# Optimization experiments

Measured on AMD Instinct MI355X. Metric: run time of the kernel, lower is better.

Reference implementation:

```python
import jax, jax.numpy as jnp
import numpy as np

B = 64
L_IN = 4001
L_CONV = 998  # (4001-10)//4 + 1
D = 1000
EPS = 1e-5


def _convlin(x, cw, cb, lw, lb):
    # x: (B,1,4001), cw: (1,1,10), lw: (1000,998)
    y = jax.lax.conv_general_dilated(
        x, cw, window_strides=(4,), padding='VALID',
        dimension_numbers=('NCH', 'OIH', 'NCH')) + cb[None, :, None]  # (B,1,998)
    y = y @ lw.T + lb  # (B,1,1000)
    return jax.nn.relu(y)


def setup_inputs() -> dict:
    key = jax.random.key(0)
    ks = jax.random.split(key, 24)
    f32 = jnp.float32
    inp = {
        'x': jax.random.normal(ks[0], (B, 1, L_IN), dtype=f32),
        'bn_gamma': jnp.ones((L_IN,), f32),
        'bn_beta': jnp.zeros((L_IN,), f32),
        'bn_mean': jax.random.normal(ks[1], (L_IN,), f32) * 0.1,
        'bn_var': jax.random.uniform(ks[2], (L_IN,), f32, 0.5, 1.5),
        'conv_w_q': jax.random.normal(ks[3], (1, 1, 10), f32) * 0.3,
        'conv_b_q': jax.random.normal(ks[4], (1,), f32) * 0.1,
        'lin_w_q': jax.random.normal(ks[5], (D, L_CONV), f32) * (1.0 / np.sqrt(L_CONV)),
        'lin_b_q': jax.random.normal(ks[6], (D,), f32) * 0.02,
        'conv_w_k': jax.random.normal(ks[7], (1, 1, 10), f32) * 0.3,
        'conv_b_k': jax.random.normal(ks[8], (1,), f32) * 0.1,
        'lin_w_k': jax.random.normal(ks[9], (D, L_CONV), f32) * (1.0 / np.sqrt(L_CONV)),
        'lin_b_k': jax.random.normal(ks[10], (D,), f32) * 0.02,
        'conv_w_v': jax.random.normal(ks[11], (1, 1, 10), f32) * 0.3,
        'conv_b_v': jax.random.normal(ks[12], (1,), f32) * 0.1,
        'lin_w_v': jax.random.normal(ks[13], (D, L_CONV), f32) * (1.0 / np.sqrt(L_CONV)),
        'lin_b_v': jax.random.normal(ks[14], (D,), f32) * 0.02,
        'in_proj_w': jax.random.normal(ks[15], (3, 1), f32),
        'in_proj_b': jax.random.normal(ks[16], (3,), f32) * 0.02,
        'out_proj_w': jax.random.normal(ks[17], (1, 1), f32),
        'out_proj_b': jax.random.normal(ks[18], (1,), f32) * 0.02,
        'out_w': jax.random.normal(ks[19], (D, D), f32) * (1.0 / np.sqrt(D)),
        'out_b': jax.random.normal(ks[20], (D,), f32) * 0.02,
    }
    return inp


def reference(x, bn_gamma, bn_beta, bn_mean, bn_var,
              conv_w_q, conv_b_q, lin_w_q, lin_b_q,
              conv_w_k, conv_b_k, lin_w_k, lin_b_k,
              conv_w_v, conv_b_v, lin_w_v, lin_b_v,
              in_proj_w, in_proj_b, out_proj_w, out_proj_b,
              out_w, out_b):
    # BatchNorm1d over last dim (eval mode, running stats); x: (B,1,4001)
    xn = (x - bn_mean[None, None, :]) * jax.lax.rsqrt(bn_var[None, None, :] + EPS)
    xn = xn * bn_gamma[None, None, :] + bn_beta[None, None, :]

    Q = _convlin(xn, conv_w_q, conv_b_q, lin_w_q, lin_b_q)[:, 0, :]  # (B,1000)
    K = _convlin(xn, conv_w_k, conv_b_k, lin_w_k, lin_b_k)[:, 0, :]
    V = _convlin(xn, conv_w_v, conv_b_v, lin_w_v, lin_b_v)[:, 0, :]

    # MHA with embed_dim=1, num_heads=1 -> scalar in-projections, scale = 1
    q = Q * in_proj_w[0, 0] + in_proj_b[0]  # (B,1000)
    k = K * in_proj_w[1, 0] + in_proj_b[1]
    v = V * in_proj_w[2, 0] + in_proj_b[2]

    scores = q[:, :, None] * k[:, None, :]  # (B,1000,1000)
    attn = jax.nn.softmax(scores, axis=-1)
    ctx = jnp.einsum('bqk,bk->bq', attn, v)  # (B,1000)
    ctx = ctx * out_proj_w[0, 0] + out_proj_b[0]

    out = ctx[:, None, :] @ out_w.T + out_b  # (B,1,1000)
    return out
```

## Files before the change

kernel.cpp:

```cpp
#include <hip/hip_runtime.h>
#include <math.h>

#define NB 64
#define LIN 4001
#define LC 998
#define ND 1000
#define EPSBN 1e-5f

#define OFF_CONVT 0u
#define OFF_P     191616u
#define OFF_Q     388224u
#define OFF_KV    452224u
#define OFF_CF    583296u

__global__ __launch_bounds__(256) void k_bnconv(
    const float* __restrict__ x,
    const float* __restrict__ g, const float* __restrict__ be,
    const float* __restrict__ mu, const float* __restrict__ va,
    const float* __restrict__ cwq, const float* __restrict__ cbq,
    const float* __restrict__ cwk, const float* __restrict__ cbk,
    const float* __restrict__ cwv, const float* __restrict__ cbv,
    float* __restrict__ convT)
{
    int j = blockIdx.x * 256 + threadIdx.x;
    int b = blockIdx.y;
    if (j >= LC) return;
    const float* xb = x + (size_t)b * LIN + 4 * j;
    float aq = 0.f, ak = 0.f, av = 0.f;
#pragma unroll
    for (int t = 0; t < 10; ++t) {
        int i = 4 * j + t;
        float s  = g[i] * rsqrtf(va[i] + EPSBN);
        float xn = (xb[t] - mu[i]) * s + be[i];
        aq = fmaf(xn, cwq[t], aq);
        ak = fmaf(xn, cwk[t], ak);
        av = fmaf(xn, cwv[t], av);
    }
    convT[((size_t)0 * LC + j) * 64 + b] = aq + cbq[0];
    convT[((size_t)1 * LC + j) * 64 + b] = ak + cbk[0];
    convT[((size_t)2 * LC + j) * 64 + b] = av + cbv[0];
}

__global__ __launch_bounds__(256) void k_lin(
    const float* __restrict__ convT,
    const float* __restrict__ lwq, const float* __restrict__ lwk,
    const float* __restrict__ lwv,
    float* __restrict__ P)
{
    __shared__ float lds[16384];
    float* ldsC = lds;
    float* ldsW = lds + 8000;
    int tid  = threadIdx.x;
    int lane = tid & 63;
    int w    = tid >> 6;
    int b0   = (lane & 7) << 3;
    int d0   = (lane >> 3) << 3;
    int dgb   = blockIdx.x * 64;
    int which = blockIdx.y;
    int chunk = blockIdx.z;
    int j0 = chunk * 125;
    int jc = (LC - j0 < 125) ? (LC - j0) : 125;
    const float* lw = (which == 0) ? lwq : ((which == 1) ? lwk : lwv);

    {
        const float4* src = (const float4*)(convT + ((size_t)which * LC + j0) * 64);
        float4* dst = (float4*)ldsC;
        for (int t = tid; t < jc * 16; t += 256) dst[t] = src[t];
    }
    for (int idx = tid; idx < 8192; idx += 256) {
        int dd = idx >> 7, jj = idx & 127;
        if (jj < 127) {
            int dg = dgb + dd;
            ldsW[dd * 127 + jj] =
                (dg < ND && jj < jc) ? lw[(size_t)dg * LC + j0 + jj] : 0.f;
        }
    }
    __syncthreads();

    float acc[8][8];
#pragma unroll
    for (int i = 0; i < 8; ++i)
#pragma unroll
        for (int jx = 0; jx < 8; ++jx) acc[i][jx] = 0.f;

    int js = w * 32;
    int je = (jc < js + 32) ? jc : (js + 32);
    for (int jj = js; jj < je; ++jj) {
        float4 c0 = *(const float4*)(ldsC + jj * 64 + b0);
        float4 c1 = *(const float4*)(ldsC + jj * 64 + b0 + 4);
        float cv[8] = {c0.x, c0.y, c0.z, c0.w, c1.x, c1.y, c1.z, c1.w};
        float wv[8];
#pragma unroll
        for (int r = 0; r < 8; ++r) wv[r] = ldsW[(d0 + r) * 127 + jj];
#pragma unroll
        for (int i = 0; i < 8; ++i)
#pragma unroll
            for (int jx = 0; jx < 8; ++jx)
                acc[i][jx] = fmaf(cv[i], wv[jx], acc[i][jx]);
    }

    __syncthreads();
    float* red = lds + w * 4096;
#pragma unroll
    for (int i = 0; i < 8; ++i) {
        *(float4*)(red + (b0 + i) * 64 + d0) =
            make_float4(acc[i][0], acc[i][1], acc[i][2], acc[i][3]);
        *(float4*)(red + (b0 + i) * 64 + d0 + 4) =
            make_float4(acc[i][4], acc[i][5], acc[i][6], acc[i][7]);
    }
    __syncthreads();
    float* Pt = P + ((size_t)(which * 16 + blockIdx.x)) * 4096;
    for (int t = tid; t < 1024; t += 256) {
        float4 a = ((const float4*)lds)[t];
        float4 bq = ((const float4*)(lds + 4096))[t];
        float4 c = ((const float4*)(lds + 8192))[t];
        float4 d = ((const float4*)(lds + 12288))[t];
        atomicAdd(Pt + t * 4 + 0, a.x + bq.x + c.x + d.x);
        atomicAdd(Pt + t * 4 + 1, a.y + bq.y + c.y + d.y);
        atomicAdd(Pt + t * 4 + 2, a.z + bq.z + c.z + d.z);
        atomicAdd(Pt + t * 4 + 3, a.w + bq.w + c.w + d.w);
    }
}

__global__ __launch_bounds__(256) void k_act(
    const float* __restrict__ P,
    const float* __restrict__ lbq, const float* __restrict__ lbk,
    const float* __restrict__ lbv,
    const float* __restrict__ ipw, const float* __restrict__ ipb,
    float* __restrict__ q, float* __restrict__ kv)
{
    int i = blockIdx.x * 256 + threadIdx.x;
    int b = blockIdx.y;
    if (i >= ND) return;
    int it = i >> 6, il = i & 63;
    size_t cell = (size_t)it * 4096 + (b << 6) + il;
    float s0 = P[(0 * 16) * 4096 + cell];
    float s1 = P[(1 * 16) * 4096 + cell];
    float s2 = P[(2 * 16) * 4096 + cell];
    float yq = fmaxf(s0 + lbq[i], 0.f) * ipw[0] + ipb[0];
    float yk = fmaxf(s1 + lbk[i], 0.f) * ipw[1] + ipb[1];
    float yv = fmaxf(s2 + lbv[i], 0.f) * ipw[2] + ipb[2];
    q[(size_t)b * ND + i] = yq;
    kv[(size_t)b * 2048 + 2 * i]     = yk;
    kv[(size_t)b * 2048 + 2 * i + 1] = yv;
}

__global__ __launch_bounds__(256) void k_attn(
    const float* __restrict__ q, const float* __restrict__ kv,
    const float* __restrict__ opw, const float* __restrict__ opb,
    float* __restrict__ cfT)
{
    __shared__ float ldsKV[2048];
    __shared__ float sred[512];
    __shared__ float rmax[4];
    __shared__ float rmin[4];
    int tid  = threadIdx.x;
    int b    = blockIdx.y;
    int half = tid >> 7;
    int ii   = tid & 127;
    int i    = blockIdx.x * 128 + ii;

    {
        const float4* src = (const float4*)(kv + (size_t)b * 2048);
        float4* dst = (float4*)ldsKV;
        for (int t = tid; t < 512; t += 256) dst[t] = src[t];
    }
    __syncthreads();

    float km = -INFINITY, kn = INFINITY;
    const float2* kv2 = (const float2*)ldsKV;
    for (int idx = tid; idx < ND; idx += 256) {
        float2 f = kv2[idx];
        km = fmaxf(km, f.x);
        kn = fminf(kn, f.x);
    }
#pragma unroll
    for (int off = 1; off < 64; off <<= 1) {
        km = fmaxf(km, __shfl_xor(km, off));
        kn = fminf(kn, __shfl_xor(kn, off));
    }
    if ((tid & 63) == 0) { rmax[tid >> 6] = km; rmin[tid >> 6] = kn; }
    __syncthreads();
    km = fmaxf(fmaxf(rmax[0], rmax[1]), fmaxf(rmax[2], rmax[3]));
    kn = fminf(fminf(rmin[0], rmin[1]), fminf(rmin[2], rmin[3]));

    float qi = (i < ND) ? q[(size_t)b * ND + i] : 0.f;
    float m  = (qi >= 0.f) ? qi * km : qi * kn;

    int jbase = half * 500;
    float den = 0.f, num = 0.f;
#pragma unroll 4
    for (int jl = 0; jl < 500; ++jl) {
        float2 f = kv2[jbase + jl];
        float e  = __expf(fmaf(qi, f.x, -m));
        den += e;
        num = fmaf(e, f.y, num);
    }
    sred[tid]       = den;
    sred[256 + tid] = num;
    __syncthreads();
    if (half == 0 && i < ND) {
        float dt  = sred[ii] + sred[128 + ii];
        float nt  = sred[256 + ii] + sred[256 + 128 + ii];
        float ctx = nt / dt;
        cfT[(size_t)i * 64 + b] = ctx * opw[0] + opb[0];
    }
}

__global__ __launch_bounds__(256) void k_out(
    const float* __restrict__ cfT, const float* __restrict__ W,
    const float* __restrict__ outb, float* __restrict__ out)
{
    __shared__ float lds[16384];
    float* ldsC = lds;
    float* ldsW = lds + 8000;
    int tid  = threadIdx.x;
    int lane = tid & 63;
    int w    = tid >> 6;
    int b0   = (lane & 7) << 3;
    int d0   = (lane >> 3) << 3;
    int egb   = blockIdx.x * 64;
    int chunk = blockIdx.y;
    int j0 = chunk * 125;

    {
        const float4* src = (const float4*)(cfT + (size_t)j0 * 64);
        float4* dst = (float4*)ldsC;
        for (int t = tid; t < 125 * 16; t += 256) dst[t] = src[t];
    }
    for (int idx = tid; idx < 8192; idx += 256) {
        int dd = idx >> 7, jj = idx & 127;
        if (jj < 127) {
            int eg = egb + dd;
            ldsW[dd * 127 + jj] =
                (eg < ND && jj < 125) ? W[(size_t)eg * ND + j0 + jj] : 0.f;
        }
    }
    __syncthreads();

    float acc[8][8];
#pragma unroll
    for (int i = 0; i < 8; ++i)
#pragma unroll
        for (int jx = 0; jx < 8; ++jx) acc[i][jx] = 0.f;

    int js = w * 32;
    int je = (125 < js + 32) ? 125 : (js + 32);
    for (int jj = js; jj < je; ++jj) {
        float4 c0 = *(const float4*)(ldsC + jj * 64 + b0);
        float4 c1 = *(const float4*)(ldsC + jj * 64 + b0 + 4);
        float cv[8] = {c0.x, c0.y, c0.z, c0.w, c1.x, c1.y, c1.z, c1.w};
        float wv[8];
#pragma unroll
        for (int r = 0; r < 8; ++r) wv[r] = ldsW[(d0 + r) * 127 + jj];
#pragma unroll
        for (int i = 0; i < 8; ++i)
#pragma unroll
            for (int jx = 0; jx < 8; ++jx)
                acc[i][jx] = fmaf(cv[i], wv[jx], acc[i][jx]);
    }

    __syncthreads();
    float* red = lds + w * 4096;
#pragma unroll
    for (int i = 0; i < 8; ++i) {
        *(float4*)(red + (b0 + i) * 64 + d0) =
            make_float4(acc[i][0], acc[i][1], acc[i][2], acc[i][3]);
        *(float4*)(red + (b0 + i) * 64 + d0 + 4) =
            make_float4(acc[i][4], acc[i][5], acc[i][6], acc[i][7]);
    }
    __syncthreads();
    for (int t = tid; t < 4096; t += 256) {
        int bb = t >> 6, dd = t & 63;
        int eg = egb + dd;
        if (eg < ND) {
            float v = lds[t] + lds[4096 + t] + lds[8192 + t] + lds[12288 + t];
            if (chunk == 0) v += outb[eg];
            atomicAdd(out + (size_t)bb * ND + eg, v);
        }
    }
}

extern "C" void kernel_launch(void* const* d_in, const int* in_sizes, int n_in,
                              void* d_out, int out_size, void* d_ws, size_t ws_size,
                              hipStream_t stream)
{
    const float* x    = (const float*)d_in[0];
    const float* g    = (const float*)d_in[1];
    const float* be   = (const float*)d_in[2];
    const float* mu   = (const float*)d_in[3];
    const float* va   = (const float*)d_in[4];
    const float* cwq  = (const float*)d_in[5];
    const float* cbq  = (const float*)d_in[6];
    const float* lwq  = (const float*)d_in[7];
    const float* lbq  = (const float*)d_in[8];
    const float* cwk  = (const float*)d_in[9];
    const float* cbk  = (const float*)d_in[10];
    const float* lwk  = (const float*)d_in[11];
    const float* lbk  = (const float*)d_in[12];
    const float* cwv  = (const float*)d_in[13];
    const float* cbv  = (const float*)d_in[14];
    const float* lwv  = (const float*)d_in[15];
    const float* lbv  = (const float*)d_in[16];
    const float* ipw  = (const float*)d_in[17];
    const float* ipb  = (const float*)d_in[18];
    const float* opw  = (const float*)d_in[19];
    const float* opb  = (const float*)d_in[20];
    const float* W    = (const float*)d_in[21];
    const float* outb = (const float*)d_in[22];

    float* ws    = (float*)d_ws;
    float* convT = ws + OFF_CONVT;
    float* P     = ws + OFF_P;
    float* q     = ws + OFF_Q;
    float* kv    = ws + OFF_KV;
    float* cfT   = ws + OFF_CF;
    float* out   = (float*)d_out;

    hipMemsetAsync(P, 0, 196608u * sizeof(float), stream);
    hipMemsetAsync(d_out, 0, (size_t)out_size * sizeof(float), stream);

    k_bnconv<<<dim3(4, 64), 256, 0, stream>>>(x, g, be, mu, va,
                                              cwq, cbq, cwk, cbk, cwv, cbv, convT);
    k_lin  <<<dim3(16, 3, 8), 256, 0, stream>>>(convT, lwq, lwk, lwv, P);
    k_act  <<<dim3(4, 64), 256, 0, stream>>>(P, lbq, lbk, lbv, ipw, ipb, q, kv);
    k_attn <<<dim3(8, 64), 256, 0, stream>>>(q, kv, opw, opb, cfT);
    k_out  <<<dim3(16, 8), 256, 0, stream>>>(cfT, W, outb, out);
}
```

Measured before the change: 197.1 us.

## Replace atomic split-K reductions with per-chunk partial buffers and finish kernels

Both GEMMs now share a tile routine that writes per-chunk partial sums to workspace instead of using atomicAdd, with the split-K chunk size lowered to 96 and the chunk count raised to 11. The bias-add and chunk sum are done in k_act and in a new k_fin kernel, so the two memsets are dropped. Weight loads are vectorised to float2, and the attention kernel splits the key loop four ways over 64 queries per block, doubling the grid. This removes atomic contention and memset launches at the cost of one extra kernel launch and more workspace traffic.

```diff
diff --git a/kernel.cpp b/kernel.cpp
--- a/kernel.cpp
+++ b/kernel.cpp
@@ -7,11 +7,16 @@
 #define ND 1000
 #define EPSBN 1e-5f
 
+#define CK 96
+#define NCH_LIN 11
+#define NCH_OUT 11
+
 #define OFF_CONVT 0u
-#define OFF_P     191616u
-#define OFF_Q     388224u
-#define OFF_KV    452224u
-#define OFF_CF    583296u
+#define OFF_PP    191616u
+#define OFF_Q     2354304u
+#define OFF_KV    2418304u
+#define OFF_CF    2549376u
+#define OFF_OP    2613376u
 
 __global__ __launch_bounds__(256) void k_bnconv(
     const float* __restrict__ x,
@@ -41,39 +46,34 @@
     convT[((size_t)2 * LC + j) * 64 + b] = av + cbv[0];
 }
 
-__global__ __launch_bounds__(256) void k_lin(
-    const float* __restrict__ convT,
-    const float* __restrict__ lwq, const float* __restrict__ lwk,
-    const float* __restrict__ lwv,
-    float* __restrict__ P)
-{
-    __shared__ float lds[16384];
+__device__ __forceinline__ void gemm_tile(
+    const float* __restrict__ Asrc,
+    const float* __restrict__ Brow,
+    int ldB, int dgb, int j0, int jc,
+    float* __restrict__ Pt,
+    float* lds)
+{
     float* ldsC = lds;
-    float* ldsW = lds + 8000;
+    float* ldsW = lds + 6144;
     int tid  = threadIdx.x;
     int lane = tid & 63;
     int w    = tid >> 6;
     int b0   = (lane & 7) << 3;
     int d0   = (lane >> 3) << 3;
-    int dgb   = blockIdx.x * 64;
-    int which = blockIdx.y;
-    int chunk = blockIdx.z;
-    int j0 = chunk * 125;
-    int jc = (LC - j0 < 125) ? (LC - j0) : 125;
-    const float* lw = (which == 0) ? lwq : ((which == 1) ? lwk : lwv);
 
     {
-        const float4* src = (const float4*)(convT + ((size_t)which * LC + j0) * 64);
+        const float4* src = (const float4*)Asrc;
         float4* dst = (float4*)ldsC;
         for (int t = tid; t < jc * 16; t += 256) dst[t] = src[t];
     }
-    for (int idx = tid; idx < 8192; idx += 256) {
-        int dd = idx >> 7, jj = idx & 127;
-        if (jj < 127) {
-            int dg = dgb + dd;
-            ldsW[dd * 127 + jj] =
-                (dg < ND && jj < jc) ? lw[(size_t)dg * LC + j0 + jj] : 0.f;
-        }
+    for (int idx = tid; idx < 3072; idx += 256) {
+        int dd = idx / 48, j2 = idx % 48;
+        int dg = dgb + dd;
+        float2 v = make_float2(0.f, 0.f);
+        if (dg < ND && 2 * j2 < jc)
+            v = *(const float2*)(Brow + (size_t)dg * ldB + j0 + 2 * j2);
+        ldsW[dd * 97 + 2 * j2]     = v.x;
+        ldsW[dd * 97 + 2 * j2 + 1] = v.y;
     }
     __syncthreads();
 
@@ -83,47 +83,68 @@
 #pragma unroll
         for (int jx = 0; jx < 8; ++jx) acc[i][jx] = 0.f;
 
-    int js = w * 32;
-    int je = (jc < js + 32) ? jc : (js + 32);
+    int js = (jc * w) >> 2;
+    int je = (jc * (w + 1)) >> 2;
     for (int jj = js; jj < je; ++jj) {
         float4 c0 = *(const float4*)(ldsC + jj * 64 + b0);
         float4 c1 = *(const float4*)(ldsC + jj * 64 + b0 + 4);
         float cv[8] = {c0.x, c0.y, c0.z, c0.w, c1.x, c1.y, c1.z, c1.w};
         float wv[8];
 #pragma unroll
-        for (int r = 0; r < 8; ++r) wv[r] = ldsW[(d0 + r) * 127 + jj];
+        for (int r = 0; r < 8; ++r) wv[r] = ldsW[(d0 + r) * 97 + jj];
 #pragma unroll
         for (int i = 0; i < 8; ++i)
 #pragma unroll
             for (int jx = 0; jx < 8; ++jx)
                 acc[i][jx] = fmaf(cv[i], wv[jx], acc[i][jx]);
     }
-
-    __syncthreads();
-    float* red = lds + w * 4096;
-#pragma unroll
-    for (int i = 0; i < 8; ++i) {
-        *(float4*)(red + (b0 + i) * 64 + d0) =
-            make_float4(acc[i][0], acc[i][1], acc[i][2], acc[i][3]);
-        *(float4*)(red + (b0 + i) * 64 + d0 + 4) =
-            make_float4(acc[i][4], acc[i][5], acc[i][6], acc[i][7]);
-    }
-    __syncthreads();
-    float* Pt = P + ((size_t)(which * 16 + blockIdx.x)) * 4096;
-    for (int t = tid; t < 1024; t += 256) {
-        float4 a = ((const float4*)lds)[t];
-        float4 bq = ((const float4*)(lds + 4096))[t];
-        float4 c = ((const float4*)(lds + 8192))[t];
-        float4 d = ((const float4*)(lds + 12288))[t];
-        atomicAdd(Pt + t * 4 + 0, a.x + bq.x + c.x + d.x);
-        atomicAdd(Pt + t * 4 + 1, a.y + bq.y + c.y + d.y);
-        atomicAdd(Pt + t * 4 + 2, a.z + bq.z + c.z + d.z);
-        atomicAdd(Pt + t * 4 + 3, a.w + bq.w + c.w + d.w);
-    }
+    __syncthreads();
+
+    for (int p = 0; p < 2; ++p) {
+        float* red = lds + w * 2304;
+#pragma unroll
+        for (int i = 0; i < 8; ++i)
+            *(float4*)(red + (b0 + i) * 36 + (d0 >> 1)) =
+                make_float4(acc[i][4*p], acc[i][4*p+1], acc[i][4*p+2], acc[i][4*p+3]);
+        __syncthreads();
+        for (int t = tid; t < 512; t += 256) {
+            int bb = t >> 3, gg = t & 7;
+            int o = bb * 36 + 4 * gg;
+            float4 a0 = *(const float4*)(lds + o);
+            float4 a1 = *(const float4*)(lds + 2304 + o);
+            float4 a2 = *(const float4*)(lds + 4608 + o);
+            float4 a3 = *(const float4*)(lds + 6912 + o);
+            float4 s;
+            s.x = a0.x + a1.x + a2.x + a3.x;
+            s.y = a0.y + a1.y + a2.y + a3.y;
+            s.z = a0.z + a1.z + a2.z + a3.z;
+            s.w = a0.w + a1.w + a2.w + a3.w;
+            *(float4*)(Pt + bb * 64 + 8 * gg + 4 * p) = s;
+        }
+        __syncthreads();
+    }
+}
+
+__global__ __launch_bounds__(256) void k_lin(
+    const float* __restrict__ convT,
+    const float* __restrict__ lwq, const float* __restrict__ lwk,
+    const float* __restrict__ lwv,
+    float* __restrict__ Pp)
+{
+    __shared__ float lds[12352];
+    int dgb   = blockIdx.x * 64;
+    int which = blockIdx.y;
+    int chunk = blockIdx.z;
+    int j0 = chunk * CK;
+    int jc = (LC - j0 < CK) ? (LC - j0) : CK;
+    const float* lw = (which == 0) ? lwq : ((which == 1) ? lwk : lwv);
+    const float* Asrc = convT + ((size_t)which * LC + j0) * 64;
+    float* Pt = Pp + (((size_t)chunk * 3 + which) * 16 + blockIdx.x) * 4096;
+    gemm_tile(Asrc, lw, LC, dgb, j0, jc, Pt, lds);
 }
 
 __global__ __launch_bounds__(256) void k_act(
-    const float* __restrict__ P,
+    const float* __restrict__ Pp,
     const float* __restrict__ lbq, const float* __restrict__ lbk,
     const float* __restrict__ lbv,
     const float* __restrict__ ipw, const float* __restrict__ ipb,
@@ -133,10 +154,13 @@
     int b = blockIdx.y;
     if (i >= ND) return;
     int it = i >> 6, il = i & 63;
-    size_t cell = (size_t)it * 4096 + (b << 6) + il;
-    float s0 = P[(0 * 16) * 4096 + cell];
-    float s1 = P[(1 * 16) * 4096 + cell];
-    float s2 = P[(2 * 16) * 4096 + cell];
+    float s0 = 0.f, s1 = 0.f, s2 = 0.f;
+    for (int c = 0; c < NCH_LIN; ++c) {
+        size_t base = (((size_t)c * 3) * 16 + it) * 4096 + (il | (b << 6));
+        s0 += Pp[base];
+        s1 += Pp[base + 16 * 4096];
+        s2 += Pp[base + 32 * 4096];
+    }
     float yq = fmaxf(s0 + lbq[i], 0.f) * ipw[0] + ipb[0];
     float yk = fmaxf(s1 + lbk[i], 0.f) * ipw[1] + ipb[1];
     float yv = fmaxf(s2 + lbv[i], 0.f) * ipw[2] + ipb[2];
@@ -151,14 +175,15 @@
     float* __restrict__ cfT)
 {
     __shared__ float ldsKV[2048];
-    __shared__ float sred[512];
+    __shared__ float sden[256];
+    __shared__ float snum[256];
     __shared__ float rmax[4];
     __shared__ float rmin[4];
-    int tid  = threadIdx.x;
-    int b    = blockIdx.y;
-    int half = tid >> 7;
-    int ii   = tid & 127;
-    int i    = blockIdx.x * 128 + ii;
+    int tid = threadIdx.x;
+    int b   = blockIdx.y;
+    int w   = tid >> 6;
+    int ii  = tid & 63;
+    int i   = blockIdx.x * 64 + ii;
 
     {
         const float4* src = (const float4*)(kv + (size_t)b * 2048);
@@ -167,8 +192,8 @@
     }
     __syncthreads();
 
+    const float2* kv2 = (const float2*)ldsKV;
     float km = -INFINITY, kn = INFINITY;
-    const float2* kv2 = (const float2*)ldsKV;
     for (int idx = tid; idx < ND; idx += 256) {
         float2 f = kv2[idx];
         km = fmaxf(km, f.x);
@@ -179,7 +204,7 @@
         km = fmaxf(km, __shfl_xor(km, off));
         kn = fminf(kn, __shfl_xor(kn, off));
     }
-    if ((tid & 63) == 0) { rmax[tid >> 6] = km; rmin[tid >> 6] = kn; }
+    if (ii == 0) { rmax[w] = km; rmin[w] = kn; }
     __syncthreads();
     km = fmaxf(fmaxf(rmax[0], rmax[1]), fmaxf(rmax[2], rmax[3]));
     kn = fminf(fminf(rmin[0], rmin[1]), fminf(rmin[2], rmin[3]));
@@ -187,98 +212,51 @@
     float qi = (i < ND) ? q[(size_t)b * ND + i] : 0.f;
     float m  = (qi >= 0.f) ? qi * km : qi * kn;
 
-    int jbase = half * 500;
+    int jb = w * 250;
     float den = 0.f, num = 0.f;
-#pragma unroll 4
-    for (int jl = 0; jl < 500; ++jl) {
-        float2 f = kv2[jbase + jl];
+#pragma unroll 2
+    for (int jl = 0; jl < 250; ++jl) {
+        float2 f = kv2[jb + jl];
         float e  = __expf(fmaf(qi, f.x, -m));
         den += e;
         num = fmaf(e, f.y, num);
     }
-    sred[tid]       = den;
-    sred[256 + tid] = num;
-    __syncthreads();
-    if (half == 0 && i < ND) {
-        float dt  = sred[ii] + sred[128 + ii];
-        float nt  = sred[256 + ii] + sred[256 + 128 + ii];
-        float ctx = nt / dt;
-        cfT[(size_t)i * 64 + b] = ctx * opw[0] + opb[0];
+    sden[tid] = den;
+    snum[tid] = num;
+    __syncthreads();
+    if (w == 0 && i < ND) {
+        float dt = sden[ii] + sden[64 + ii] + sden[128 + ii] + sden[192 + ii];
+        float nt = snum[ii] + snum[64 + ii] + snum[128 + ii] + snum[192 + ii];
+        cfT[(size_t)i * 64 + b] = (nt / dt) * opw[0] + opb[0];
     }
 }
 
 __global__ __launch_bounds__(256) void k_out(
     const float* __restrict__ cfT, const float* __restrict__ W,
-    const float* __restrict__ outb, float* __restrict__ out)
-{
-    __shared__ float lds[16384];
-    float* ldsC = lds;
-    float* ldsW = lds + 8000;
-    int tid  = threadIdx.x;
-    int lane = tid & 63;
-    int w    = tid >> 6;
-    int b0   = (lane & 7) << 3;
-    int d0   = (lane >> 3) << 3;
+    float* __restrict__ Op)
+{
+    __shared__ float lds[12352];
     int egb   = blockIdx.x * 64;
     int chunk = blockIdx.y;
-    int j0 = chunk * 125;
-
-    {
-        const float4* src = (const float4*)(cfT + (size_t)j0 * 64);
-        float4* dst = (float4*)ldsC;
-        for (int t = tid; t < 125 * 16; t += 256) dst[t] = src[t];
-    }
-    for (int idx = tid; idx < 8192; idx += 256) {
-        int dd = idx >> 7, jj = idx & 127;
-        if (jj < 127) {
-            int eg = egb + dd;
-            ldsW[dd * 127 + jj] =
-                (eg < ND && jj < 125) ? W[(size_t)eg * ND + j0 + jj] : 0.f;
-        }
-    }
-    __syncthreads();
-
-    float acc[8][8];
-#pragma unroll
-    for (int i = 0; i < 8; ++i)
-#pragma unroll
-        for (int jx = 0; jx < 8; ++jx) acc[i][jx] = 0.f;
-
-    int js = w * 32;
-    int je = (125 < js + 32) ? 125 : (js + 32);
-    for (int jj = js; jj < je; ++jj) {
-        float4 c0 = *(const float4*)(ldsC + jj * 64 + b0);
-        float4 c1 = *(const float4*)(ldsC + jj * 64 + b0 + 4);
-        float cv[8] = {c0.x, c0.y, c0.z, c0.w, c1.x, c1.y, c1.z, c1.w};
-        float wv[8];
-#pragma unroll
-        for (int r = 0; r < 8; ++r) wv[r] = ldsW[(d0 + r) * 127 + jj];
-#pragma unroll
-        for (int i = 0; i < 8; ++i)
-#pragma unroll
-            for (int jx = 0; jx < 8; ++jx)
-                acc[i][jx] = fmaf(cv[i], wv[jx], acc[i][jx]);
-    }
-
-    __syncthreads();
-    float* red = lds + w * 4096;
-#pragma unroll
-    for (int i = 0; i < 8; ++i) {
-        *(float4*)(red + (b0 + i) * 64 + d0) =
-            make_float4(acc[i][0], acc[i][1], acc[i][2], acc[i][3]);
-        *(float4*)(red + (b0 + i) * 64 + d0 + 4) =
-            make_float4(acc[i][4], acc[i][5], acc[i][6], acc[i][7]);
-    }
-    __syncthreads();
-    for (int t = tid; t < 4096; t += 256) {
-        int bb = t >> 6, dd = t & 63;
-        int eg = egb + dd;
-        if (eg < ND) {
-            float v = lds[t] + lds[4096 + t] + lds[8192 + t] + lds[12288 + t];
-            if (chunk == 0) v += outb[eg];
-            atomicAdd(out + (size_t)bb * ND + eg, v);
-        }
-    }
+    int j0 = chunk * CK;
+    int jc = (ND - j0 < CK) ? (ND - j0) : CK;
+    const float* Asrc = cfT + (size_t)j0 * 64;
+    float* Pt = Op + ((size_t)chunk * 16 + blockIdx.x) * 4096;
+    gemm_tile(Asrc, W, ND, egb, j0, jc, Pt, lds);
+}
+
+__global__ __launch_bounds__(256) void k_fin(
+    const float* __restrict__ Op, const float* __restrict__ outb,
+    float* __restrict__ out)
+{
+    int e = blockIdx.x * 256 + threadIdx.x;
+    int b = blockIdx.y;
+    if (e >= ND) return;
+    float s = outb[e];
+    size_t cell = ((size_t)(e >> 6)) * 4096 + (b << 6) + (e & 63);
+    for (int c = 0; c < NCH_OUT; ++c)
+        s += Op[(size_t)c * 16 * 4096 + cell];
+    out[(size_t)b * ND + e] = s;
 }
 
 extern "C" void kernel_launch(void* const* d_in, const int* in_sizes, int n_in,
@@ -311,19 +289,18 @@
 
     float* ws    = (float*)d_ws;
     float* convT = ws + OFF_CONVT;
-    float* P     = ws + OFF_P;
+    float* Pp    = ws + OFF_PP;
     float* q     = ws + OFF_Q;
     float* kv    = ws + OFF_KV;
     float* cfT   = ws + OFF_CF;
+    float* Op    = ws + OFF_OP;
     float* out   = (float*)d_out;
-
-    hipMemsetAsync(P, 0, 196608u * sizeof(float), stream);
-    hipMemsetAsync(d_out, 0, (size_t)out_size * sizeof(float), stream);
 
     k_bnconv<<<dim3(4, 64), 256, 0, stream>>>(x, g, be, mu, va,
                                               cwq, cbq, cwk, cbk, cwv, cbv, convT);
-    k_lin  <<<dim3(16, 3, 8), 256, 0, stream>>>(convT, lwq, lwk, lwv, P);
-    k_act  <<<dim3(4, 64), 256, 0, stream>>>(P, lbq, lbk, lbv, ipw, ipb, q, kv);
-    k_attn <<<dim3(8, 64), 256, 0, stream>>>(q, kv, opw, opb, cfT);
-    k_out  <<<dim3(16, 8), 256, 0, stream>>>(cfT, W, outb, out);
-}
+    k_lin  <<<dim3(16, 3, NCH_LIN), 256, 0, stream>>>(convT, lwq, lwk, lwv, Pp);
+    k_act  <<<dim3(4, 64), 256, 0, stream>>>(Pp, lbq, lbk, lbv, ipw, ipb, q, kv);
+    k_attn <<<dim3(16, 64), 256, 0, stream>>>(q, kv, opw, opb, cfT);
+    k_out  <<<dim3(16, NCH_OUT), 256, 0, stream>>>(cfT, W, Op);
+    k_fin  <<<dim3(4, 64), 256, 0, stream>>>(Op, outb, out);
+}
```

After: 166.3 us. 15.6% less time.
